# Performance work log

Hardware: AMD Instinct MI355X
Metric: run time of the kernel (lower is better)

Reference implementation:

```python
import jax, jax.numpy as jnp
import numpy as np

N = 100000       # nodes
DEG = 16         # fixed out/in degree used to build CSR
E = N * DEG      # edges
D_IN = 128       # in_feats
D_OUT = 256      # out_feats
K = 32           # maxk k_value


def _xavier_uniform(key, shape, gain):
    fan_out, fan_in = shape
    bound = gain * np.sqrt(6.0 / (fan_in + fan_out))
    return jax.random.uniform(key, shape, jnp.float32, -bound, bound)


def setup_inputs() -> dict:
    key = jax.random.key(0)
    ks = jax.random.split(key, 6)
    feat = jax.random.normal(ks[0], (N, D_IN), jnp.float32)
    topk_values = jax.random.uniform(ks[1], (N, K), jnp.float32)
    topk_indices = jax.random.randint(ks[2], (N, K), 0, D_IN).astype(jnp.int32)
    # CSR graph: fixed degree -> indptr is arange*DEG; random destinations
    indptr = (jnp.arange(N + 1) * DEG).astype(jnp.int32)
    indices = jax.random.randint(ks[3], (E,), 0, N).astype(jnp.int32)
    # set_graph_data: csr weight[e] = 1 / clamp(in_degree(dst), 1)
    in_deg = jax.ops.segment_sum(jnp.ones(E, jnp.float32), indices, num_segments=N)
    in_deg = jnp.maximum(in_deg, 1.0)
    csr_values = 1.0 / in_deg[indices]
    gain = np.sqrt(2.0)  # calculate_gain('relu')
    w_neigh = _xavier_uniform(ks[4], (D_OUT, D_IN), gain)
    w_self = _xavier_uniform(ks[5], (D_OUT, D_IN), gain)
    b_self = jnp.zeros((D_OUT,), jnp.float32)
    return {"feat": feat, "topk_values": topk_values, "csr_values": csr_values,
            "w_neigh": w_neigh, "w_self": w_self, "b_self": b_self,
            "topk_indices": topk_indices, "indptr": indptr, "indices": indices}


def reference(feat, topk_values, csr_values, w_neigh, w_self, b_self,
              topk_indices, indptr, indices):
    # Densify the k-sparse MaxK features: x[n, topk_indices[n, j]] = topk_values[n, j]
    x = jnp.zeros((N, D_IN), feat.dtype).at[
        jnp.arange(N)[:, None], topk_indices].add(topk_values)
    # Edge-weight-normalized SpMM over CSR: out[row] += w[e] * x[col[e]]
    row_ids = jnp.repeat(jnp.arange(N), jnp.diff(indptr), total_repeat_length=E)
    msgs = x[indices] * csr_values[:, None]          # [E, D_IN]
    agg = jax.ops.segment_sum(msgs, row_ids, num_segments=N)  # [N, D_IN]
    # lin_before_mp is False (in_feats <= out_feats): project after aggregation
    h_neigh = agg @ w_neigh.T                        # [N, D_OUT]
    rst = feat @ w_self.T + b_self + h_neigh         # fc_self(h_self) + h_neigh
    return rst
```

## Files before the change

### kernel.cpp

```cpp
#include <hip/hip_runtime.h>
#include <hip/hip_bf16.h>
#include <stdint.h>

#define N_NODES 100000
#define DEG 16
#define D_IN 128
#define D_OUT 256
#define K_TOP 32
#define K_CAT 256

typedef __attribute__((ext_vector_type(8))) short short8;
typedef __attribute__((ext_vector_type(4))) float floatx4;

__device__ __forceinline__ unsigned pack_bf16_rne(float f) {
    union { float f; unsigned u; } c; c.f = f;
    unsigned u = c.u;
    return (u + 0x7fffu + ((u >> 16) & 1u)) >> 16;
}
__device__ __forceinline__ float bf16lo_to_f(unsigned lo16) {
    union { unsigned u; float f; } c; c.u = lo16 << 16; return c.f;
}

__global__ __launch_bounds__(256) void k_packw(const float* __restrict__ w_self,
                                               const float* __restrict__ w_neigh,
                                               unsigned short* __restrict__ bmat) {
    int o = blockIdx.x;
    int k = threadIdx.x;
    float v = (k < D_IN) ? w_self[o * D_IN + k] : w_neigh[o * D_IN + (k - D_IN)];
    bmat[o * K_CAT + k] = (unsigned short)pack_bf16_rne(v);
}

#define DROWS 64
__global__ __launch_bounds__(256) void k_densify(const float* __restrict__ topk_v,
                                                 const int* __restrict__ topk_i,
                                                 const float* __restrict__ feat,
                                                 unsigned short* __restrict__ xbf,
                                                 unsigned short* __restrict__ abf) {
    __shared__ float sx[DROWS * D_IN];
    const int t = threadIdx.x;
    const int row0 = blockIdx.x * DROWS;

    #pragma unroll
    for (int p = 0; p < 8; ++p)
        *(floatx4*)&sx[(t + p * 256) * 4] = (floatx4){0.f, 0.f, 0.f, 0.f};
    __syncthreads();

    const size_t tbase = (size_t)row0 * K_TOP;
    #pragma unroll
    for (int p = 0; p < 8; ++p) {
        int q = t + p * 256;
        int r = q >> 5;
        if (row0 + r < N_NODES) {
            int   ci = topk_i[tbase + q];
            float cv = topk_v[tbase + q];
            atomicAdd(&sx[r * D_IN + ci], cv);
        }
    }
    __syncthreads();

    #pragma unroll
    for (int p = 0; p < 16; ++p) {
        int d = t + p * 256;
        int r = d >> 6;
        int c2 = (d & 63) * 2;
        if (row0 + r < N_NODES) {
            float2 v = *(const float2*)&sx[r * D_IN + c2];
            ((unsigned*)(xbf + (size_t)(row0 + r) * D_IN))[d & 63] =
                pack_bf16_rne(v.x) | (pack_bf16_rne(v.y) << 16);
        }
    }

    #pragma unroll
    for (int p = 0; p < 8; ++p) {
        int q = t + p * 256;
        int r = q >> 5;
        int c4 = (q & 31) * 4;
        if (row0 + r < N_NODES) {
            float4 f = *(const float4*)(feat + (size_t)(row0 + r) * D_IN + c4);
            uint2 pk;
            pk.x = pack_bf16_rne(f.x) | (pack_bf16_rne(f.y) << 16);
            pk.y = pack_bf16_rne(f.z) | (pack_bf16_rne(f.w) << 16);
            ((uint2*)(abf + (size_t)(row0 + r) * K_CAT))[q & 31] = pk;
        }
    }
}

__global__ __launch_bounds__(256) void k_spmm(const float* __restrict__ csr_w,
                                              const int* __restrict__ col_idx,
                                              const unsigned short* __restrict__ xbf,
                                              unsigned short* __restrict__ abf) {
    const int wave = threadIdx.x >> 6;
    const int lane = threadIdx.x & 63;
    const int pair = blockIdx.x * 4 + wave;
    const int row  = 2 * pair + (lane >> 5);
    const int hl   = lane & 31;
    if (row >= N_NODES) return;

    int c = 0; float w = 0.f;
    if (hl < DEG) {
        c = col_idx[row * DEG + hl];
        w = csr_w[row * DEG + hl];
    }
    const int bsel = lane & 32;
    uint2 vv[DEG];
    #pragma unroll
    for (int e = 0; e < DEG; ++e) {
        int col = __shfl(c, bsel | e);
        vv[e] = *(const uint2*)(xbf + (size_t)col * D_IN + hl * 4);
    }
    float a0 = 0.f, a1 = 0.f, a2 = 0.f, a3 = 0.f;
    #pragma unroll
    for (int e = 0; e < DEG; ++e) {
        float we = __shfl(w, bsel | e);
        a0 += we * bf16lo_to_f(vv[e].x & 0xffffu);
        a1 += we * bf16lo_to_f(vv[e].x >> 16);
        a2 += we * bf16lo_to_f(vv[e].y & 0xffffu);
        a3 += we * bf16lo_to_f(vv[e].y >> 16);
    }
    uint2 pk;
    pk.x = pack_bf16_rne(a0) | (pack_bf16_rne(a1) << 16);
    pk.y = pack_bf16_rne(a2) | (pack_bf16_rne(a3) << 16);
    ((uint2*)(abf + (size_t)row * K_CAT + D_IN))[hl] = pk;
}

#define BM 128
#define BN 256
#define BK 32
#define LDP 40

__global__ __launch_bounds__(256, 2) void k_gemm(const unsigned short* __restrict__ abf,
                                                 const unsigned short* __restrict__ bmat,
                                                 const float* __restrict__ bias,
                                                 float* __restrict__ out) {
    __shared__ unsigned short As[BM * LDP];
    __shared__ unsigned short Bs[BN * LDP];
    int t = threadIdx.x;
    int lane = t & 63, wave = t >> 6;
    int wr = wave >> 1, wc = wave & 1;
    int row0 = blockIdx.x * BM;

    floatx4 acc[4][8];
    #pragma unroll
    for (int i = 0; i < 4; ++i)
        #pragma unroll
        for (int j = 0; j < 8; ++j)
            acc[i][j] = (floatx4){0.f, 0.f, 0.f, 0.f};

    int quad = lane >> 4;
    int l16  = lane & 15;

    for (int kt = 0; kt < K_CAT; kt += BK) {
        __syncthreads();
        #pragma unroll
        for (int p = 0; p < 2; ++p) {
            int chunk = t + p * 256;
            int r  = chunk >> 2;
            int ko = (chunk & 3) * 8;
            uint4 av = make_uint4(0u, 0u, 0u, 0u);
            int gr = row0 + r;
            if (gr < N_NODES)
                av = *(const uint4*)(abf + (size_t)gr * K_CAT + kt + ko);
            *(uint4*)&As[r * LDP + ko] = av;
        }
        #pragma unroll
        for (int p = 0; p < 4; ++p) {
            int chunk = t + p * 256;
            int r  = chunk >> 2;
            int ko = (chunk & 3) * 8;
            uint4 bv = *(const uint4*)(bmat + (size_t)r * K_CAT + kt + ko);
            *(uint4*)&Bs[r * LDP + ko] = bv;
        }
        __syncthreads();

        short8 afr[4], bfr[8];
        #pragma unroll
        for (int i = 0; i < 4; ++i) {
            int m = wr * 64 + i * 16 + l16;
            afr[i] = *(const short8*)&As[m * LDP + quad * 8];
        }
        #pragma unroll
        for (int j = 0; j < 8; ++j) {
            int n = wc * 128 + j * 16 + l16;
            bfr[j] = *(const short8*)&Bs[n * LDP + quad * 8];
        }
        #pragma unroll
        for (int i = 0; i < 4; ++i)
            #pragma unroll
            for (int j = 0; j < 8; ++j)
                acc[i][j] = __builtin_amdgcn_mfma_f32_16x16x32_bf16(afr[i], bfr[j], acc[i][j], 0, 0, 0);
    }

    #pragma unroll
    for (int j = 0; j < 8; ++j) {
        int cg = wc * 128 + j * 16 + l16;
        float bv = bias[cg];
        #pragma unroll
        for (int i = 0; i < 4; ++i) {
            int mbase = row0 + wr * 64 + i * 16 + quad * 4;
            #pragma unroll
            for (int r = 0; r < 4; ++r) {
                int gr = mbase + r;
                if (gr < N_NODES) out[(size_t)gr * D_OUT + cg] = acc[i][j][r] + bv;
            }
        }
    }
}

extern "C" void kernel_launch(void* const* d_in, const int* in_sizes, int n_in,
                              void* d_out, int out_size, void* d_ws, size_t ws_size,
                              hipStream_t stream) {
    const float* feat    = (const float*)d_in[0];
    const float* topk_v  = (const float*)d_in[1];
    const float* csr_w   = (const float*)d_in[2];
    const float* w_neigh = (const float*)d_in[3];
    const float* w_self  = (const float*)d_in[4];
    const float* b_self  = (const float*)d_in[5];
    const int*   topk_i  = (const int*)d_in[6];
    const int*   indices = (const int*)d_in[8];
    float* out = (float*)d_out;

    unsigned short* xbf  = (unsigned short*)d_ws;
    unsigned short* abf  = xbf + (size_t)N_NODES * D_IN;
    unsigned short* bmat = abf + (size_t)N_NODES * K_CAT;

    k_packw<<<dim3(256), dim3(256), 0, stream>>>(w_self, w_neigh, bmat);
    k_densify<<<dim3((N_NODES + DROWS - 1) / DROWS), dim3(256), 0, stream>>>(topk_v, topk_i, feat, xbf, abf);
    k_spmm<<<dim3((N_NODES + 7) / 8), dim3(256), 0, stream>>>(csr_w, indices, xbf, abf);
    k_gemm<<<dim3((N_NODES + BM - 1) / BM), dim3(256), 0, stream>>>(abf, bmat, b_self, out);
}
```

Before: 304.1 us.

## Rework SpMM to 16-byte gathers and GEMM to double-buffered direct-to-LDS loads

The SpMM kernel now handles four rows per wave with 16 lanes each, gathering 16-byte chunks instead of 8-byte ones, which halves the number of gather instructions per row. The GEMM switches to 128x128 output tiles split across two column blocks for more blocks and higher occupancy. It stages A and B with global_load_lds straight into double-buffered, unpadded shared memory and drops one barrier per K step. The MFMA operands are swapped so each lane holds four consecutive output columns, allowing float4 stores of the output. Risks are LDS bank conflicts from removing the padding and re-reading A once per column tile.

After: 302.5 us. About the same (-0.5%).

```diff
diff --git a/kernel.cpp b/kernel.cpp
--- a/kernel.cpp
+++ b/kernel.cpp
@@ -19,6 +19,12 @@
 }
 __device__ __forceinline__ float bf16lo_to_f(unsigned lo16) {
     union { unsigned u; float f; } c; c.u = lo16 << 16; return c.f;
+}
+
+typedef __attribute__((address_space(1))) void as1_void;
+typedef __attribute__((address_space(3))) void as3_void;
+__device__ __forceinline__ void gload_lds16(const void* g, void* l) {
+    __builtin_amdgcn_global_load_lds((as1_void*)g, (as3_void*)l, 16, 0, 0);
 }
 
 __global__ __launch_bounds__(256) void k_packw(const float* __restrict__ w_self,
@@ -89,121 +95,126 @@
                                               const int* __restrict__ col_idx,
                                               const unsigned short* __restrict__ xbf,
                                               unsigned short* __restrict__ abf) {
+    const int lane = threadIdx.x & 63;
     const int wave = threadIdx.x >> 6;
-    const int lane = threadIdx.x & 63;
-    const int pair = blockIdx.x * 4 + wave;
-    const int row  = 2 * pair + (lane >> 5);
-    const int hl   = lane & 31;
-    if (row >= N_NODES) return;
-
-    int c = 0; float w = 0.f;
-    if (hl < DEG) {
-        c = col_idx[row * DEG + hl];
-        w = csr_w[row * DEG + hl];
-    }
-    const int bsel = lane & 32;
-    uint2 vv[DEG];
+    const int ql   = lane & 15;
+    const int row  = blockIdx.x * 16 + wave * 4 + (lane >> 4);
+    const int qb   = lane & 48;
+
+    int   c = col_idx[row * DEG + ql];
+    float w = csr_w[row * DEG + ql];
+
+    uint4 vv[DEG];
     #pragma unroll
     for (int e = 0; e < DEG; ++e) {
-        int col = __shfl(c, bsel | e);
-        vv[e] = *(const uint2*)(xbf + (size_t)col * D_IN + hl * 4);
-    }
-    float a0 = 0.f, a1 = 0.f, a2 = 0.f, a3 = 0.f;
+        int col = __shfl(c, qb | e);
+        vv[e] = *(const uint4*)(xbf + (size_t)col * D_IN + ql * 8);
+    }
+    float a[8] = {0.f, 0.f, 0.f, 0.f, 0.f, 0.f, 0.f, 0.f};
     #pragma unroll
     for (int e = 0; e < DEG; ++e) {
-        float we = __shfl(w, bsel | e);
-        a0 += we * bf16lo_to_f(vv[e].x & 0xffffu);
-        a1 += we * bf16lo_to_f(vv[e].x >> 16);
-        a2 += we * bf16lo_to_f(vv[e].y & 0xffffu);
-        a3 += we * bf16lo_to_f(vv[e].y >> 16);
-    }
-    uint2 pk;
-    pk.x = pack_bf16_rne(a0) | (pack_bf16_rne(a1) << 16);
-    pk.y = pack_bf16_rne(a2) | (pack_bf16_rne(a3) << 16);
-    ((uint2*)(abf + (size_t)row * K_CAT + D_IN))[hl] = pk;
+        float we = __shfl(w, qb | e);
+        uint4 v = vv[e];
+        a[0] += we * bf16lo_to_f(v.x & 0xffffu);
+        a[1] += we * bf16lo_to_f(v.x >> 16);
+        a[2] += we * bf16lo_to_f(v.y & 0xffffu);
+        a[3] += we * bf16lo_to_f(v.y >> 16);
+        a[4] += we * bf16lo_to_f(v.z & 0xffffu);
+        a[5] += we * bf16lo_to_f(v.z >> 16);
+        a[6] += we * bf16lo_to_f(v.w & 0xffffu);
+        a[7] += we * bf16lo_to_f(v.w >> 16);
+    }
+    uint4 pk;
+    pk.x = pack_bf16_rne(a[0]) | (pack_bf16_rne(a[1]) << 16);
+    pk.y = pack_bf16_rne(a[2]) | (pack_bf16_rne(a[3]) << 16);
+    pk.z = pack_bf16_rne(a[4]) | (pack_bf16_rne(a[5]) << 16);
+    pk.w = pack_bf16_rne(a[6]) | (pack_bf16_rne(a[7]) << 16);
+    *(uint4*)(abf + (size_t)row * K_CAT + D_IN + ql * 8) = pk;
 }
 
 #define BM 128
-#define BN 256
+#define BN 128
 #define BK 32
-#define LDP 40
-
-__global__ __launch_bounds__(256, 2) void k_gemm(const unsigned short* __restrict__ abf,
+#define NT (K_CAT / BK)
+
+__global__ __launch_bounds__(256, 4) void k_gemm(const unsigned short* __restrict__ abf,
                                                  const unsigned short* __restrict__ bmat,
                                                  const float* __restrict__ bias,
                                                  float* __restrict__ out) {
-    __shared__ unsigned short As[BM * LDP];
-    __shared__ unsigned short Bs[BN * LDP];
-    int t = threadIdx.x;
-    int lane = t & 63, wave = t >> 6;
-    int wr = wave >> 1, wc = wave & 1;
-    int row0 = blockIdx.x * BM;
-
-    floatx4 acc[4][8];
+    __shared__ __align__(16) unsigned short As[2][BM * BK];
+    __shared__ __align__(16) unsigned short Bs[2][BN * BK];
+    const int lane = threadIdx.x & 63, wave = threadIdx.x >> 6;
+    const int wr = wave >> 1, wc = wave & 1;
+    const int l16 = lane & 15, quad = lane >> 4;
+    const int rt = blockIdx.x >> 1, ct = blockIdx.x & 1;
+    const int row0 = rt * BM, n0 = ct * BN;
+
+    const int sr = wave * 32 + (lane >> 2);
+    const int sc = (lane & 3) * 8;
+    int arow0 = row0 + sr;      if (arow0 >= N_NODES) arow0 = N_NODES - 1;
+    int arow1 = row0 + sr + 16; if (arow1 >= N_NODES) arow1 = N_NODES - 1;
+    const int brow0 = n0 + sr, brow1 = n0 + sr + 16;
+    const unsigned short* ga0 = abf  + (size_t)arow0 * K_CAT + sc;
+    const unsigned short* ga1 = abf  + (size_t)arow1 * K_CAT + sc;
+    const unsigned short* gb0 = bmat + (size_t)brow0 * K_CAT + sc;
+    const unsigned short* gb1 = bmat + (size_t)brow1 * K_CAT + sc;
+
+#define STAGE(buf, kt) do {                                                  \
+        gload_lds16(ga0 + (kt), &As[buf][(wave * 32)      * BK]);            \
+        gload_lds16(ga1 + (kt), &As[buf][(wave * 32 + 16) * BK]);            \
+        gload_lds16(gb0 + (kt), &Bs[buf][(wave * 32)      * BK]);            \
+        gload_lds16(gb1 + (kt), &Bs[buf][(wave * 32 + 16) * BK]);            \
+    } while (0)
+
+    floatx4 acc[4][4];
     #pragma unroll
     for (int i = 0; i < 4; ++i)
         #pragma unroll
-        for (int j = 0; j < 8; ++j)
+        for (int j = 0; j < 4; ++j)
             acc[i][j] = (floatx4){0.f, 0.f, 0.f, 0.f};
 
-    int quad = lane >> 4;
-    int l16  = lane & 15;
-
-    for (int kt = 0; kt < K_CAT; kt += BK) {
-        __syncthreads();
-        #pragma unroll
-        for (int p = 0; p < 2; ++p) {
-            int chunk = t + p * 256;
-            int r  = chunk >> 2;
-            int ko = (chunk & 3) * 8;
-            uint4 av = make_uint4(0u, 0u, 0u, 0u);
-            int gr = row0 + r;
-            if (gr < N_NODES)
-                av = *(const uint4*)(abf + (size_t)gr * K_CAT + kt + ko);
-            *(uint4*)&As[r * LDP + ko] = av;
-        }
-        #pragma unroll
-        for (int p = 0; p < 4; ++p) {
-            int chunk = t + p * 256;
-            int r  = chunk >> 2;
-            int ko = (chunk & 3) * 8;
-            uint4 bv = *(const uint4*)(bmat + (size_t)r * K_CAT + kt + ko);
-            *(uint4*)&Bs[r * LDP + ko] = bv;
-        }
-        __syncthreads();
-
-        short8 afr[4], bfr[8];
-        #pragma unroll
-        for (int i = 0; i < 4; ++i) {
-            int m = wr * 64 + i * 16 + l16;
-            afr[i] = *(const short8*)&As[m * LDP + quad * 8];
-        }
-        #pragma unroll
-        for (int j = 0; j < 8; ++j) {
-            int n = wc * 128 + j * 16 + l16;
-            bfr[j] = *(const short8*)&Bs[n * LDP + quad * 8];
-        }
+    STAGE(0, 0);
+    __syncthreads();
+
+    for (int t8 = 0; t8 < NT; ++t8) {
+        const int cur = t8 & 1;
+        if (t8 + 1 < NT) STAGE(cur ^ 1, (t8 + 1) * BK);
+
+        short8 afr[4], bfr[4];
+        #pragma unroll
+        for (int i = 0; i < 4; ++i)
+            afr[i] = *(const short8*)&As[cur][(wr * 64 + i * 16 + l16) * BK + quad * 8];
+        #pragma unroll
+        for (int j = 0; j < 4; ++j)
+            bfr[j] = *(const short8*)&Bs[cur][(wc * 64 + j * 16 + l16) * BK + quad * 8];
+
         #pragma unroll
         for (int i = 0; i < 4; ++i)
             #pragma unroll
-            for (int j = 0; j < 8; ++j)
-                acc[i][j] = __builtin_amdgcn_mfma_f32_16x16x32_bf16(afr[i], bfr[j], acc[i][j], 0, 0, 0);
-    }
-
-    #pragma unroll
-    for (int j = 0; j < 8; ++j) {
-        int cg = wc * 128 + j * 16 + l16;
-        float bv = bias[cg];
+            for (int j = 0; j < 4; ++j)
+                acc[i][j] = __builtin_amdgcn_mfma_f32_16x16x32_bf16(bfr[j], afr[i], acc[i][j], 0, 0, 0);
+
+        if (t8 + 1 < NT) __syncthreads();
+    }
+
+    #pragma unroll
+    for (int j = 0; j < 4; ++j) {
+        const int cg = n0 + wc * 64 + j * 16 + quad * 4;
+        const float4 bv = *(const float4*)&bias[cg];
         #pragma unroll
         for (int i = 0; i < 4; ++i) {
-            int mbase = row0 + wr * 64 + i * 16 + quad * 4;
-            #pragma unroll
-            for (int r = 0; r < 4; ++r) {
-                int gr = mbase + r;
-                if (gr < N_NODES) out[(size_t)gr * D_OUT + cg] = acc[i][j][r] + bv;
+            const int gr = row0 + wr * 64 + i * 16 + l16;
+            if (gr < N_NODES) {
+                float4 v;
+                v.x = acc[i][j][0] + bv.x;
+                v.y = acc[i][j][1] + bv.y;
+                v.z = acc[i][j][2] + bv.z;
+                v.w = acc[i][j][3] + bv.w;
+                *(float4*)(out + (size_t)gr * D_OUT + cg) = v;
             }
         }
     }
+#undef STAGE
 }
 
 extern "C" void kernel_launch(void* const* d_in, const int* in_sizes, int n_in,
@@ -225,6 +236,6 @@
 
     k_packw<<<dim3(256), dim3(256), 0, stream>>>(w_self, w_neigh, bmat);
     k_densify<<<dim3((N_NODES + DROWS - 1) / DROWS), dim3(256), 0, stream>>>(topk_v, topk_i, feat, xbf, abf);
-    k_spmm<<<dim3((N_NODES + 7) / 8), dim3(256), 0, stream>>>(csr_w, indices, xbf, abf);
-    k_gemm<<<dim3((N_NODES + BM - 1) / BM), dim3(256), 0, stream>>>(abf, bmat, b_self, out);
-}
+    k_spmm<<<dim3(N_NODES / 16), dim3(256), 0, stream>>>(csr_w, indices, xbf, abf);
+    k_gemm<<<dim3(2 * ((N_NODES + BM - 1) / BM)), dim3(256), 0, stream>>>(abf, bmat, b_self, out);
+}
```
